# Kernel optimization log

Measured on AMD Instinct MI355X. Metric: run time of the kernel, lower is better.

## Reference

```python
import jax, jax.numpy as jnp
import numpy as np

CUTOFF = 8.0
N_NODES = 100000
N_EDGES = 3200000
HIDDEN = 256
VOCAB = 178


def _swish(x):
    return x * jax.nn.sigmoid(x)


def _safe_norm(v):
    # L2 norm over last axis with torch-style zero subgradient at 0
    ss = jnp.sum(v * v, axis=-1)
    return jnp.where(ss == 0, 0.0, jnp.sqrt(jnp.where(ss == 0, 1.0, ss)))


def _safe_atan2(b, a):
    # atan2 with finite grad at (0,0); forward value identical (atan2(0,0)=0)
    deg = (a == 0) & (b == 0)
    return jnp.arctan2(b, jnp.where(deg, 1.0, a))


def _scatter_argmin(d, idx, num_seg):
    # replicates torch_scatter.scatter_min argmin output (empty segments -> 0)
    E = d.shape[0]
    mn = jax.ops.segment_min(d, idx, num_segments=num_seg)
    cand = jnp.where(d == mn[idx], jnp.arange(E), E)
    am = jax.ops.segment_min(cand, idx, num_segments=num_seg)
    return jnp.where(am >= E, 0, am)


def _dist_calc(cutoff, vecs, dist, i, j, num_nodes):
    argmin0 = _scatter_argmin(dist, i, num_nodes)
    n0 = j[argmin0]
    dist1 = dist + jnp.zeros_like(dist).at[argmin0].set(cutoff)
    argmin1 = _scatter_argmin(dist1, i, num_nodes)
    n1 = j[argmin1]
    argmin0_j = _scatter_argmin(dist, j, num_nodes)
    n0_j = i[argmin0_j]
    dist1_j = dist + jnp.zeros_like(dist).at[argmin0_j].set(cutoff)
    argmin1_j = _scatter_argmin(dist1_j, j, num_nodes)
    n1_j = i[argmin1_j]

    n0 = n0[i]
    n1 = n1[i]
    n0_j = n0_j[j]
    n1_j = n1_j[j]

    idx_iref = jnp.where(n0 == j, argmin1[i], argmin0[i])
    idx_jref = jnp.where(n0_j == i, argmin1_j[j], argmin0_j[j])

    pos_ji = vecs                      # [E,3]
    pos_in0 = vecs[argmin0[i]]         # vecs[argmin0][i]
    pos_in1 = vecs[argmin1[i]]
    pos_iref = vecs[idx_iref]
    pos_jref_j = vecs[idx_jref]

    a = jnp.sum(-pos_ji * pos_in0, axis=-1)
    b = _safe_norm(jnp.cross(-pos_ji, pos_in0))
    theta = _safe_atan2(b, a)
    theta = jnp.where(theta < 0, theta + jnp.pi, theta)

    dist_ji = _safe_norm(pos_ji)

    plane1 = jnp.cross(-pos_ji, pos_in0)
    plane2 = jnp.cross(-pos_ji, pos_in1)
    a = jnp.sum(plane1 * plane2, axis=-1)
    b = jnp.sum(jnp.cross(plane1, plane2) * pos_ji, axis=-1) / dist_ji
    phi = _safe_atan2(b, a)
    phi = jnp.where(phi < 0, phi + jnp.pi, phi)

    plane1 = jnp.cross(pos_ji, pos_jref_j)
    plane2 = jnp.cross(pos_ji, pos_iref)
    a = jnp.sum(plane1 * plane2, axis=-1)
    b = jnp.sum(jnp.cross(plane1, plane2) * pos_ji, axis=-1) / dist_ji
    tau = _safe_atan2(b, a)
    tau = jnp.where(tau < 0, tau + jnp.pi, tau)

    return dist, theta, phi, tau


def setup_inputs() -> dict:
    key = jax.random.key(0)
    k1, k2, k3, k4, k5 = jax.random.split(key, 5)
    x = jax.random.randint(k1, (N_NODES,), 0, VOCAB)
    pos = jax.random.normal(k2, (N_NODES, 3), jnp.float32) * 3.0
    i = jax.random.randint(k3, (N_EDGES,), 0, N_NODES)
    off = jax.random.randint(k4, (N_EDGES,), 1, N_NODES)
    j = (i + off) % N_NODES  # no self-edges -> dist > 0
    edge_index = jnp.stack([i, j])
    emb_weight = jax.random.normal(k5, (VOCAB, HIDDEN), jnp.float32)
    return {"x": x, "pos": pos, "edge_index": edge_index, "emb_weight": emb_weight}


def reference(x, pos, edge_index, emb_weight):
    i, j = edge_index[0], edge_index[1]
    vecs = pos[j] - pos[i]          # [E,3]
    dist = _safe_norm(vecs)         # [E]
    h = _swish(emb_weight[x])       # [N,H]
    dist, theta, phi, tau = _dist_calc(CUTOFF, vecs, dist, i, j, pos.shape[0])
    return h, dist, theta, phi, tau
```

## Files before the change

kernel.cpp:

```cpp
#include <hip/hip_runtime.h>
#include <math.h>

#define HID 256
#define PI_F 3.14159265358979323846f
typedef unsigned long long ull;

struct F3 { float x, y, z; };

__device__ __forceinline__ F3 crossc(F3 a, F3 b) {
    F3 r;
    float t1 = a.z * b.y;
    r.x = __builtin_fmaf(a.y, b.z, -t1);
    float t2 = a.x * b.z;
    r.y = __builtin_fmaf(a.z, b.x, -t2);
    float t3 = a.y * b.x;
    r.z = __builtin_fmaf(a.x, b.y, -t3);
    return r;
}
__device__ __forceinline__ float dotf(F3 a, F3 b) {
#pragma clang fp contract(off)
    float px = a.x * b.x;
    float py = a.y * b.y;
    float pz = a.z * b.z;
    return (px + py) + pz;
}
__device__ __forceinline__ float sqrt_cr(float ss) {
    return (float)sqrt((double)ss);
}
__device__ __forceinline__ float safe_atan2(float b, float a) {
    float aa = (a == 0.f && b == 0.f) ? 1.f : a;
    return atan2f(b, aa);
}
__device__ __forceinline__ F3 loadp(const float* __restrict__ pos, int n) {
    F3 r;
    r.x = pos[3 * n + 0];
    r.y = pos[3 * n + 1];
    r.z = pos[3 * n + 2];
    return r;
}
__device__ __forceinline__ F3 subv(F3 a, F3 b) {
#pragma clang fp contract(off)
    F3 r;
    r.x = a.x - b.x;
    r.y = a.y - b.y;
    r.z = a.z - b.z;
    return r;
}
__device__ __forceinline__ ull umin64(ull a, ull b) { return a < b ? a : b; }
__device__ __forceinline__ ull umax64(ull a, ull b) { return a > b ? a : b; }

__device__ __forceinline__ void insert2(ull* __restrict__ s, unsigned db, ull key) {
    unsigned hi2 = ((const unsigned*)s)[3];
    if (db > hi2) return;
    unsigned hi1 = ((const unsigned*)s)[1];
    if (db <= hi1) {
        ull ret = atomicMin(&s[0], key);
        ull loser = umax64(ret, key);
        if (loser != ~0ull) atomicMin(&s[1], loser);
    } else {
        atomicMin(&s[1], key);
    }
}

__global__ void k_pass1(const int* __restrict__ ei, const int* __restrict__ ej,
                        const float* __restrict__ pos, float* __restrict__ dist,
                        ull* __restrict__ slotsA, ull* __restrict__ slotsB, int E) {
#pragma clang fp contract(off)
    int e = blockIdx.x * blockDim.x + threadIdx.x;
    if (e >= E) return;
    int ii = ei[e], jj = ej[e];
    F3 v = subv(loadp(pos, jj), loadp(pos, ii));
    float sx = v.x * v.x;
    float sy = v.y * v.y;
    float sz = v.z * v.z;
    float ss = (sx + sy) + sz;
    float d = (ss == 0.f) ? 0.f : sqrt_cr(ss);
    dist[e] = d;
    unsigned db = __float_as_uint(d);
    ull key = ((ull)db << 32) | (unsigned)e;
    insert2(&slotsA[2 * (size_t)ii], db, key);
    insert2(&slotsB[2 * (size_t)jj], db, key);
}

__global__ void k_prep(const ull* __restrict__ slotsA, const ull* __restrict__ slotsB,
                       const int* __restrict__ ei, const int* __restrict__ ej,
                       const float* __restrict__ pos,
                       float4* __restrict__ nodeI, float4* __restrict__ nodeJ,
                       int* __restrict__ a0i, int* __restrict__ a0j,
                       unsigned* __restrict__ flags, int N) {
#pragma clang fp contract(off)
    int n = blockIdx.x * blockDim.x + threadIdx.x;
    if (n >= N) return;

    ull k1 = slotsA[2 * (size_t)n];
    int a0, a1;
    if (k1 == ~0ull) {
        a0 = 0; a1 = 0;
        atomicOr(&flags[0], 1u);
    } else {
        a0 = (int)(k1 & 0xffffffffu);
        float d0 = __uint_as_float((unsigned)(k1 >> 32));
        ull mkey = ((ull)__float_as_uint(d0 + 8.0f) << 32) | (unsigned)a0;
        ull k2 = slotsA[2 * (size_t)n + 1];
        if (k2 == ~0ull) a1 = a0;
        else a1 = (mkey < k2) ? a0 : (int)(k2 & 0xffffffffu);
    }
    a0i[n] = a0;
    F3 in0 = subv(loadp(pos, ej[a0]), loadp(pos, ei[a0]));
    int n0 = ej[a0];
    F3 in1 = subv(loadp(pos, ej[a1]), loadp(pos, ei[a1]));
    nodeI[2 * (size_t)n]     = make_float4(in0.x, in0.y, in0.z, __int_as_float(n0));
    nodeI[2 * (size_t)n + 1] = make_float4(in1.x, in1.y, in1.z, 0.f);

    ull q1 = slotsB[2 * (size_t)n];
    int b0, b1;
    if (q1 == ~0ull) {
        b0 = 0; b1 = 0;
        atomicOr(&flags[1], 1u);
    } else {
        b0 = (int)(q1 & 0xffffffffu);
        float d0 = __uint_as_float((unsigned)(q1 >> 32));
        ull mkey = ((ull)__float_as_uint(d0 + 8.0f) << 32) | (unsigned)b0;
        ull q2 = slotsB[2 * (size_t)n + 1];
        if (q2 == ~0ull) b1 = b0;
        else b1 = (mkey < q2) ? b0 : (int)(q2 & 0xffffffffu);
    }
    a0j[n] = b0;
    F3 w0 = subv(loadp(pos, ej[b0]), loadp(pos, ei[b0]));
    int m0 = ei[b0];
    F3 w1 = subv(loadp(pos, ej[b1]), loadp(pos, ei[b1]));
    nodeJ[2 * (size_t)n]     = make_float4(w0.x, w0.y, w0.z, __int_as_float(m0));
    nodeJ[2 * (size_t)n + 1] = make_float4(w1.x, w1.y, w1.z, 0.f);
}

__global__ void k_fix(const unsigned* __restrict__ flags,
                      const int* __restrict__ ei, const int* __restrict__ ej,
                      const float* __restrict__ dist,
                      const int* __restrict__ a0i, const int* __restrict__ a0j,
                      const float* __restrict__ pos,
                      float4* __restrict__ nodeI, float4* __restrict__ nodeJ, int E) {
#pragma clang fp contract(off)
    __shared__ ull smin[256];
    int side = blockIdx.x;
    if (flags[side] == 0u) return;
    const int* seg = (side == 0) ? ei : ej;
    int s = seg[0];
    int marked = (side == 0) ? a0i[s] : a0j[s];
    ull local = ~0ull;
    for (int e = threadIdx.x; e < E; e += 256) {
        if (seg[e] != s) continue;
        float d = dist[e];
        float dm = (e == marked || e == 0) ? (d + 8.0f) : d;
        ull key = ((ull)__float_as_uint(dm) << 32) | (unsigned)e;
        local = umin64(local, key);
    }
    smin[threadIdx.x] = local;
    __syncthreads();
    for (int w = 128; w > 0; w >>= 1) {
        if (threadIdx.x < w) smin[threadIdx.x] = umin64(smin[threadIdx.x], smin[threadIdx.x + w]);
        __syncthreads();
    }
    if (threadIdx.x == 0) {
        int a1 = (smin[0] == ~0ull) ? 0 : (int)(smin[0] & 0xffffffffu);
        F3 v = subv(loadp(pos, ej[a1]), loadp(pos, ei[a1]));
        if (side == 0) nodeI[2 * (size_t)s + 1] = make_float4(v.x, v.y, v.z, 0.f);
        else           nodeJ[2 * (size_t)s + 1] = make_float4(v.x, v.y, v.z, 0.f);
    }
}

__global__ void k_angles(const int* __restrict__ ei, const int* __restrict__ ej,
                         const float* __restrict__ pos, const float* __restrict__ dist,
                         const float4* __restrict__ nodeI, const float4* __restrict__ nodeJ,
                         float* __restrict__ theta, float* __restrict__ phi,
                         float* __restrict__ tau, int E) {
    int e = blockIdx.x * blockDim.x + threadIdx.x;
    if (e >= E) return;
    int ii = ei[e], jj = ej[e];

    float4 A0 = nodeI[2 * (size_t)ii];
    float4 A1 = nodeI[2 * (size_t)ii + 1];
    float4 B0 = nodeJ[2 * (size_t)jj];
    float4 B1 = nodeJ[2 * (size_t)jj + 1];
    int n0 = __float_as_int(A0.w);
    int m0 = __float_as_int(B0.w);

    F3 in0; in0.x = A0.x; in0.y = A0.y; in0.z = A0.z;
    F3 in1; in1.x = A1.x; in1.y = A1.y; in1.z = A1.z;
    F3 w0;  w0.x = B0.x;  w0.y = B0.y;  w0.z = B0.z;
    F3 w1;  w1.x = B1.x;  w1.y = B1.y;  w1.z = B1.z;

    F3 iref = (n0 == jj) ? in1 : in0;
    F3 jref = (m0 == ii) ? w1 : w0;

    F3 p = subv(loadp(pos, jj), loadp(pos, ii));
    F3 mp;
    mp.x = -p.x; mp.y = -p.y; mp.z = -p.z;

    float a = dotf(mp, in0);
    F3 c1 = crossc(mp, in0);
    float ssb = dotf(c1, c1);
    float b = (ssb == 0.f) ? 0.f : sqrt_cr(ssb);
    float th = safe_atan2(b, a);
    if (th < 0.f) th += PI_F;

    float dji = dist[e];

    F3 pl2 = crossc(mp, in1);
    a = dotf(c1, pl2);
    F3 cc = crossc(c1, pl2);
    b = dotf(cc, p) / dji;
    float ph = safe_atan2(b, a);
    if (ph < 0.f) ph += PI_F;

    F3 t1 = crossc(p, jref);
    F3 t2 = crossc(p, iref);
    a = dotf(t1, t2);
    cc = crossc(t1, t2);
    b = dotf(cc, p) / dji;
    float ta = safe_atan2(b, a);
    if (ta < 0.f) ta += PI_F;

    theta[e] = th;
    phi[e] = ph;
    tau[e] = ta;
}

__global__ void k_embed(const int* __restrict__ x, const float* __restrict__ w,
                        float* __restrict__ h, int total4) {
    int t = blockIdx.x * blockDim.x + threadIdx.x;
    if (t >= total4) return;
    int n = t >> 6;
    int c = t & 63;
    int row = x[n];
    float4 v = *reinterpret_cast<const float4*>(w + (size_t)row * HID + c * 4);
    float4 o;
    o.x = v.x / (1.f + expf(-v.x));
    o.y = v.y / (1.f + expf(-v.y));
    o.z = v.z / (1.f + expf(-v.z));
    o.w = v.w / (1.f + expf(-v.w));
    *reinterpret_cast<float4*>(h + (size_t)n * HID + c * 4) = o;
}

extern "C" void kernel_launch(void* const* d_in, const int* in_sizes, int n_in,
                              void* d_out, int out_size, void* d_ws, size_t ws_size,
                              hipStream_t stream) {
    const int* x = (const int*)d_in[0];
    const float* pos = (const float*)d_in[1];
    const int* eidx = (const int*)d_in[2];
    const float* emb = (const float*)d_in[3];

    const int N = in_sizes[0];
    const int E = in_sizes[2] / 2;
    const int* ei = eidx;
    const int* ej = eidx + E;

    float* out = (float*)d_out;
    float* out_h = out;
    float* out_dist = out + (size_t)N * HID;
    float* out_theta = out_dist + E;
    float* out_phi = out_theta + E;
    float* out_tau = out_phi + E;

    ull* slotsA = (ull*)out_h;
    ull* slotsB = slotsA + 2 * (size_t)N;
    float4* nodeI = (float4*)(slotsB + 2 * (size_t)N);
    float4* nodeJ = nodeI + 2 * (size_t)N;
    int* a0i = (int*)(nodeJ + 2 * (size_t)N);
    int* a0j = a0i + N;
    unsigned* flags = (unsigned*)(a0j + N);

    const int BS = 256;
    int gE = (E + BS - 1) / BS;
    int gN = (N + BS - 1) / BS;
    int total4 = N * (HID / 4);
    int gH = (total4 + BS - 1) / BS;

    hipMemsetAsync(slotsA, 0xFF, 4 * (size_t)N * sizeof(ull), stream);
    hipMemsetAsync(flags, 0, 2 * sizeof(unsigned), stream);

    k_pass1<<<gE, BS, 0, stream>>>(ei, ej, pos, out_dist, slotsA, slotsB, E);
    k_prep<<<gN, BS, 0, stream>>>(slotsA, slotsB, ei, ej, pos,
                                  nodeI, nodeJ, a0i, a0j, flags, N);
    k_fix<<<2, BS, 0, stream>>>(flags, ei, ej, out_dist, a0i, a0j, pos,
                                nodeI, nodeJ, E);
    k_angles<<<gE, BS, 0, stream>>>(ei, ej, pos, out_dist, nodeI, nodeJ,
                                    out_theta, out_phi, out_tau, E);
    k_embed<<<gH, BS, 0, stream>>>(x, emb, out_h, total4);
}
```

Measured before the change: 410.5 us.

## Chunk edge pass and filter slot inserts with snapshotted per-node thresholds

Splits the distance/argmin edge pass into five geometrically growing chunks. Between chunks, a small kernel snapshots each node's current second-best distance into compact threshold arrays. Later chunks check these thresholds before touching the atomic slot structures. This aims to cut random slot reads and atomics for edges that cannot enter the top-2, but it adds extra kernel launches and snapshot passes. The existing in-slot early exit already uses a fresher value, so the new filter may save little.

Result: faster. 388.3 us (-5.4%).

```diff
diff --git a/kernel.cpp b/kernel.cpp
--- a/kernel.cpp
+++ b/kernel.cpp
@@ -64,10 +64,12 @@
 
 __global__ void k_pass1(const int* __restrict__ ei, const int* __restrict__ ej,
                         const float* __restrict__ pos, float* __restrict__ dist,
-                        ull* __restrict__ slotsA, ull* __restrict__ slotsB, int E) {
-#pragma clang fp contract(off)
-    int e = blockIdx.x * blockDim.x + threadIdx.x;
-    if (e >= E) return;
+                        ull* __restrict__ slotsA, ull* __restrict__ slotsB,
+                        const unsigned* __restrict__ thrA, const unsigned* __restrict__ thrB,
+                        int e0, int e1) {
+#pragma clang fp contract(off)
+    int e = e0 + blockIdx.x * blockDim.x + threadIdx.x;
+    if (e >= e1) return;
     int ii = ei[e], jj = ej[e];
     F3 v = subv(loadp(pos, jj), loadp(pos, ii));
     float sx = v.x * v.x;
@@ -78,8 +80,16 @@
     dist[e] = d;
     unsigned db = __float_as_uint(d);
     ull key = ((ull)db << 32) | (unsigned)e;
-    insert2(&slotsA[2 * (size_t)ii], db, key);
-    insert2(&slotsB[2 * (size_t)jj], db, key);
+    if (db <= thrA[ii]) insert2(&slotsA[2 * (size_t)ii], db, key);
+    if (db <= thrB[jj]) insert2(&slotsB[2 * (size_t)jj], db, key);
+}
+
+__global__ void k_snapshot(const ull* __restrict__ slotsA, const ull* __restrict__ slotsB,
+                           unsigned* __restrict__ thrA, unsigned* __restrict__ thrB, int N) {
+    int n = blockIdx.x * blockDim.x + threadIdx.x;
+    if (n >= N) return;
+    thrA[n] = (unsigned)(slotsA[2 * (size_t)n + 1] >> 32);
+    thrB[n] = (unsigned)(slotsB[2 * (size_t)n + 1] >> 32);
 }
 
 __global__ void k_prep(const ull* __restrict__ slotsA, const ull* __restrict__ slotsB,
@@ -263,27 +273,39 @@
 
     ull* slotsA = (ull*)out_h;
     ull* slotsB = slotsA + 2 * (size_t)N;
-    float4* nodeI = (float4*)(slotsB + 2 * (size_t)N);
+    unsigned* thrA = (unsigned*)(slotsB + 2 * (size_t)N);
+    unsigned* thrB = thrA + N;
+    float4* nodeI = (float4*)(thrB + N);
     float4* nodeJ = nodeI + 2 * (size_t)N;
     int* a0i = (int*)(nodeJ + 2 * (size_t)N);
     int* a0j = a0i + N;
     unsigned* flags = (unsigned*)(a0j + N);
 
     const int BS = 256;
-    int gE = (E + BS - 1) / BS;
     int gN = (N + BS - 1) / BS;
     int total4 = N * (HID / 4);
     int gH = (total4 + BS - 1) / BS;
 
-    hipMemsetAsync(slotsA, 0xFF, 4 * (size_t)N * sizeof(ull), stream);
+    hipMemsetAsync(slotsA, 0xFF, 4 * (size_t)N * sizeof(ull) + 2 * (size_t)N * sizeof(unsigned), stream);
     hipMemsetAsync(flags, 0, 2 * sizeof(unsigned), stream);
 
-    k_pass1<<<gE, BS, 0, stream>>>(ei, ej, pos, out_dist, slotsA, slotsB, E);
+    int c0 = 0, c1 = E / 16, c2 = E / 8, c3 = E / 4, c4 = E / 2, c5 = E;
+    int bounds[6] = {c0, c1, c2, c3, c4, c5};
+    for (int k = 0; k < 5; k++) {
+        int lo = bounds[k], hi = bounds[k + 1];
+        if (hi <= lo) continue;
+        int g = (hi - lo + BS - 1) / BS;
+        k_pass1<<<g, BS, 0, stream>>>(ei, ej, pos, out_dist, slotsA, slotsB,
+                                      thrA, thrB, lo, hi);
+        if (k < 4)
+            k_snapshot<<<gN, BS, 0, stream>>>(slotsA, slotsB, thrA, thrB, N);
+    }
+
     k_prep<<<gN, BS, 0, stream>>>(slotsA, slotsB, ei, ej, pos,
                                   nodeI, nodeJ, a0i, a0j, flags, N);
     k_fix<<<2, BS, 0, stream>>>(flags, ei, ej, out_dist, a0i, a0j, pos,
                                 nodeI, nodeJ, E);
-    k_angles<<<gE, BS, 0, stream>>>(ei, ej, pos, out_dist, nodeI, nodeJ,
-                                    out_theta, out_phi, out_tau, E);
+    k_angles<<<(E + BS - 1) / BS, BS, 0, stream>>>(ei, ej, pos, out_dist, nodeI, nodeJ,
+                                                   out_theta, out_phi, out_tau, E);
     k_embed<<<gH, BS, 0, stream>>>(x, emb, out_h, total4);
 }
```
